# Kernel tuning notes

Hardware: AMD Instinct MI355X
Metric: run time of the kernel (lower is better)

The kernel has to match this reference:

```python
import jax, jax.numpy as jnp
import numpy as np

N = 100000
E = 1600000
IN_C, HID_C, OUT_C = 128, 64, 40


def setup_inputs() -> dict:
    key = jax.random.key(0)
    ks = jax.random.split(key, 9)
    x = jax.random.normal(ks[0], (N, IN_C), dtype=jnp.float32)
    src = jax.random.randint(ks[1], (E,), 0, N, dtype=jnp.int64)
    dst = jax.random.randint(ks[2], (E,), 0, N, dtype=jnp.int64)
    edge_index = jnp.stack([src, dst], axis=0)
    def glorot(k, fan_in, fan_out):
        s = jnp.sqrt(6.0 / (fan_in + fan_out)).astype(jnp.float32)
        return jax.random.uniform(k, (fan_in, fan_out), jnp.float32, -s, s)
    return {
        "x": x,
        "edge_index": edge_index,
        "W1": glorot(ks[3], IN_C, HID_C), "b1": jnp.zeros((HID_C,), jnp.float32),
        "W2": glorot(ks[4], HID_C, HID_C), "b2": jnp.zeros((HID_C,), jnp.float32),
        "W3": glorot(ks[5], HID_C, OUT_C), "b3": jnp.zeros((OUT_C,), jnp.float32),
    }


def _gcn_norm(edge_index, n_nodes):
    # add self-loops, then symmetric normalization D^-1/2 (A+I) D^-1/2
    loops = jnp.arange(n_nodes, dtype=edge_index.dtype)
    src = jnp.concatenate([edge_index[0], loops])
    dst = jnp.concatenate([edge_index[1], loops])
    deg = jax.ops.segment_sum(jnp.ones_like(dst, dtype=jnp.float32), dst,
                              num_segments=n_nodes)
    dinv = jnp.where(deg > 0, jax.lax.rsqrt(deg), 0.0)
    norm = dinv[src] * dinv[dst]  # [E + N]
    return src, dst, norm


def _gcn_conv(h, W, b, src, dst, norm, n_nodes):
    h = h @ W                                   # [N, out]
    msg = norm[:, None] * h[src]                # gather + scale, [E+N, out]
    out = jax.ops.segment_sum(msg, dst, num_segments=n_nodes)  # scatter-add
    return out + b


def reference(x, edge_index, W1, b1, W2, b2, W3, b3):
    n_nodes = x.shape[0]
    src, dst, norm = _gcn_norm(edge_index, n_nodes)
    h = jax.nn.relu(_gcn_conv(x, W1, b1, src, dst, norm, n_nodes))
    # dropout(p=0.5) is identity in eval mode
    h = jax.nn.relu(_gcn_conv(h, W2, b2, src, dst, norm, n_nodes))
    out = _gcn_conv(h, W3, b3, src, dst, norm, n_nodes)
    return out
```

## Files before the change

### kernel.cpp

```cpp
#include <hip/hip_runtime.h>

#define N_NODES 100000
#define N_EDGES 1600000
#define NBUCK 196
#define BCAP 9600
#define CH 4096
#define NCHUNK ((N_EDGES + CH - 1) / CH)

typedef __attribute__((ext_vector_type(2))) _Float16 half2v;
typedef __attribute__((ext_vector_type(4))) _Float16 half4v;

__device__ __forceinline__ float4 f4add(float4 a, float4 b) {
    return make_float4(a.x + b.x, a.y + b.y, a.z + b.z, a.w + b.w);
}
__device__ __forceinline__ float4 f4acch(float4 a, half4v v) {
    a.x += (float)v.x; a.y += (float)v.y; a.z += (float)v.z; a.w += (float)v.w;
    return a;
}


__global__ __launch_bounds__(256) void zero_small(int* p, int n) {
    int i = blockIdx.x * blockDim.x + threadIdx.x;
    if (i < n) p[i] = 0;
}

__global__ __launch_bounds__(256) void multisplit(const int* __restrict__ src,
                                                  const int* __restrict__ dst,
                                                  int* cursor,
                                                  int* __restrict__ bucketed, int e) {
    __shared__ int cnt[NBUCK];
    __shared__ int basel[NBUCK];
    const int t = threadIdx.x;
    const int base_e = blockIdx.x * CH;

    int myS[16], myD[16];
    for (int i = t; i < NBUCK; i += 256) cnt[i] = 0;
    __syncthreads();

#pragma unroll
    for (int k = 0; k < 16; ++k) {
        int i = base_e + k * 256 + t;
        if (i < e) {
            myS[k] = src[i];
            myD[k] = dst[i];
            atomicAdd(&cnt[myD[k] >> 9], 1);
        } else {
            myD[k] = -1;
        }
    }
    __syncthreads();
    for (int i = t; i < NBUCK; i += 256) basel[i] = atomicAdd(&cursor[i], cnt[i]);
    __syncthreads();
    for (int i = t; i < NBUCK; i += 256) cnt[i] = 0;
    __syncthreads();

#pragma unroll
    for (int k = 0; k < 16; ++k) {
        if (myD[k] >= 0) {
            int b = myD[k] >> 9;
            int pos = basel[b] + atomicAdd(&cnt[b], 1);
            if (pos < BCAP)
                bucketed[(size_t)b * BCAP + pos] = ((myD[k] & 511) << 17) | myS[k];
        }
    }
}

__global__ __launch_bounds__(256) void bucket_scan(const int* __restrict__ cursor,
                                                   int* __restrict__ gbase) {
    __shared__ int sm[256];
    const int t = threadIdx.x;
    int v = (t < NBUCK) ? cursor[t] : 0;
    sm[t] = v;
    __syncthreads();
    for (int off = 1; off < 256; off <<= 1) {
        int u = (t >= off) ? sm[t - off] : 0;
        __syncthreads();
        sm[t] += u;
        __syncthreads();
    }
    if (t < NBUCK) gbase[t] = sm[t] - v;
    if (t == NBUCK - 1) gbase[NBUCK] = sm[t];
}

__global__ __launch_bounds__(512) void build_csr(const int* __restrict__ bucketed,
                                                 const int* __restrict__ gbase,
                                                 int* __restrict__ row_ptr,
                                                 float* __restrict__ dinv,
                                                 int* __restrict__ csr_src, int n) {
    __shared__ int vals[BCAP];
    __shared__ int cnt[512];
    __shared__ int lcur[512];
    const int b = blockIdx.x;
    const int t = threadIdx.x;
    const int nb0 = b * 512;
    const int nn = min(512, n - nb0);
    const int gb = gbase[b];
    const int m = gbase[b + 1] - gb;

    cnt[t] = 0;
    __syncthreads();
    for (int i = t; i < m; i += 512) {
        int v = bucketed[(size_t)b * BCAP + i];
        vals[i] = v;
        atomicAdd(&cnt[v >> 17], 1);
    }
    __syncthreads();

    int deg = cnt[t];
    for (int off = 1; off < 512; off <<= 1) {
        int u = (t >= off) ? cnt[t - off] : 0;
        __syncthreads();
        cnt[t] += u;
        __syncthreads();
    }
    int offv = cnt[t] - deg;
    __syncthreads();
    cnt[t] = offv;
    lcur[t] = 0;
    if (t < nn) {
        row_ptr[nb0 + t] = gb + offv;
        dinv[nb0 + t] = rsqrtf((float)(deg + 1));
    }
    if (b == NBUCK - 1 && t == 0) row_ptr[n] = gb + m;
    __syncthreads();

    for (int i = t; i < m; i += 512) {
        int v = vals[i];
        int node = v >> 17;
        int pos = atomicAdd(&lcur[node], 1);
        csr_src[gb + cnt[node] + pos] = v & 0x1FFFF;
    }
}


template <int K, int COUT>
__global__ __launch_bounds__(256) void gemm_rt(const float* __restrict__ X,
                                               const float* __restrict__ W,
                                               const float* __restrict__ dinv,
                                               _Float16* __restrict__ Y, int n) {
    constexpr int KC = 64;
    constexpr int S = KC + 4;
    constexpr int NCHUNKK = K / KC;
    __shared__ float Xl[64 * S];
    __shared__ float Wl[KC * COUT];

    const int t = threadIdx.x;
    const int row0 = blockIdx.x * 64;
    const int cg = (t & 15) * 4;
    const int rg = (t >> 4) * 4;

    float acc[4][4] = {};

#pragma unroll
    for (int ch = 0; ch < NCHUNKK; ++ch) {
        const int k0 = ch * KC;
        for (int i = t; i < 64 * KC / 4; i += 256) {
            int r = i >> 4;
            int k = (i & 15) * 4;
            int grow = min(row0 + r, n - 1);
            *(float4*)(Xl + r * S + k) = *(const float4*)(X + (size_t)grow * K + k0 + k);
        }
        for (int i = t; i < KC * COUT / 4; i += 256) {
            *(float4*)(Wl + i * 4) = *(const float4*)(W + (size_t)k0 * COUT + (size_t)i * 4);
        }
        __syncthreads();

        if (cg < COUT) {
#pragma unroll 4
            for (int k = 0; k < KC; ++k) {
                float4 w = *(const float4*)(Wl + k * COUT + cg);
                float x0 = Xl[(rg + 0) * S + k];
                float x1 = Xl[(rg + 1) * S + k];
                float x2 = Xl[(rg + 2) * S + k];
                float x3 = Xl[(rg + 3) * S + k];
                acc[0][0] += x0 * w.x; acc[0][1] += x0 * w.y; acc[0][2] += x0 * w.z; acc[0][3] += x0 * w.w;
                acc[1][0] += x1 * w.x; acc[1][1] += x1 * w.y; acc[1][2] += x1 * w.z; acc[1][3] += x1 * w.w;
                acc[2][0] += x2 * w.x; acc[2][1] += x2 * w.y; acc[2][2] += x2 * w.z; acc[2][3] += x2 * w.w;
                acc[3][0] += x3 * w.x; acc[3][1] += x3 * w.y; acc[3][2] += x3 * w.z; acc[3][3] += x3 * w.w;
            }
        }
        __syncthreads();
    }

    if (cg < COUT) {
#pragma unroll
        for (int r = 0; r < 4; ++r) {
            int row = row0 + rg + r;
            if (row < n) {
                float d = dinv[row];
                half4v o = { (_Float16)(d * acc[r][0]), (_Float16)(d * acc[r][1]),
                             (_Float16)(d * acc[r][2]), (_Float16)(d * acc[r][3]) };
                *(half4v*)(Y + (size_t)row * COUT + cg) = o;
            }
        }
    }
}


template <bool RELU>
__global__ __launch_bounds__(256) void aggregate64v(const _Float16* __restrict__ tS,
                                                    const int* __restrict__ row_ptr,
                                                    const int* __restrict__ csr_src,
                                                    const float* __restrict__ dinv,
                                                    const float* __restrict__ bias,
                                                    float* __restrict__ out, int n) {
    const int lane = threadIdx.x & 63;
    const int node = blockIdx.x * 4 + (threadIdx.x >> 6);
    if (node >= n) return;
    const int g = lane >> 4;
    const int c4 = lane & 15;
    const half4v* tS4 = (const half4v*)tS;

    const int beg = row_ptr[node];
    const int cnt = row_ptr[node + 1] - beg;

    float4 a0 = {0,0,0,0}, a1 = {0,0,0,0}, a2 = {0,0,0,0}, a3 = {0,0,0,0};

    for (int j0 = 0; j0 < cnt; j0 += 64) {
        const int m = min(64, cnt - j0);
        int sj = (lane < m) ? csr_src[beg + j0 + lane] : 0;

        int j = 0;
        for (; j + 16 <= m; j += 16) {
            int e0 = __shfl(sj, j + g);
            int e1 = __shfl(sj, j + 4 + g);
            int e2 = __shfl(sj, j + 8 + g);
            int e3 = __shfl(sj, j + 12 + g);
            half4v v0 = tS4[(size_t)e0 * 16 + c4];
            half4v v1 = tS4[(size_t)e1 * 16 + c4];
            half4v v2 = tS4[(size_t)e2 * 16 + c4];
            half4v v3 = tS4[(size_t)e3 * 16 + c4];
            a0 = f4acch(a0, v0); a1 = f4acch(a1, v1);
            a2 = f4acch(a2, v2); a3 = f4acch(a3, v3);
        }
        for (; j + 4 <= m; j += 4) {
            int e0 = __shfl(sj, j + g);
            half4v v0 = tS4[(size_t)e0 * 16 + c4];
            a0 = f4acch(a0, v0);
        }
        if (j < m) {
            int idx = j + g;
            int e0 = __shfl(sj, idx < m ? idx : m - 1);
            half4v v = tS4[(size_t)e0 * 16 + c4];
            if (idx < m) a0 = f4acch(a0, v);
        }
    }

    float4 s = f4add(f4add(a0, a1), f4add(a2, a3));
#pragma unroll
    for (int off = 16; off < 64; off <<= 1) {
        s.x += __shfl_xor(s.x, off);
        s.y += __shfl_xor(s.y, off);
        s.z += __shfl_xor(s.z, off);
        s.w += __shfl_xor(s.w, off);
    }

    if (lane < 16) {
        half4v selfh = tS4[(size_t)node * 16 + c4];
        float4 b = ((const float4*)bias)[c4];
        float d = dinv[node];
        float4 o;
        o.x = b.x + d * (s.x + (float)selfh.x);
        o.y = b.y + d * (s.y + (float)selfh.y);
        o.z = b.z + d * (s.z + (float)selfh.z);
        o.w = b.w + d * (s.w + (float)selfh.w);
        if (RELU) {
            o.x = fmaxf(o.x, 0.f); o.y = fmaxf(o.y, 0.f);
            o.z = fmaxf(o.z, 0.f); o.w = fmaxf(o.w, 0.f);
        }
        ((float4*)out)[(size_t)node * 16 + c4] = o;
    }
}


__global__ __launch_bounds__(256) void aggregate40v(const _Float16* __restrict__ tS,
                                                    const int* __restrict__ row_ptr,
                                                    const int* __restrict__ csr_src,
                                                    const float* __restrict__ dinv,
                                                    const float* __restrict__ bias,
                                                    float* __restrict__ out, int n) {
    const int lane = threadIdx.x & 63;
    const int node = blockIdx.x * 4 + (threadIdx.x >> 6);
    if (node >= n) return;
    const int g = lane / 20;
    const int c2 = lane - 20 * g;
    const bool act = (g < 3);
    const half2v* tS2 = (const half2v*)tS;

    const int beg = row_ptr[node];
    const int cnt = row_ptr[node + 1] - beg;

    float2 a0 = {0,0}, a1 = {0,0}, a2 = {0,0}, a3 = {0,0};

    for (int j0 = 0; j0 < cnt; j0 += 64) {
        const int m = min(64, cnt - j0);
        int sj = (lane < m) ? csr_src[beg + j0 + lane] : 0;

        int j = 0;
        for (; j + 12 <= m; j += 12) {
            int i0 = j + g, i1 = j + 3 + g, i2 = j + 6 + g, i3 = j + 9 + g;
            int e0 = __shfl(sj, i0 < m ? i0 : 0);
            int e1 = __shfl(sj, i1 < m ? i1 : 0);
            int e2 = __shfl(sj, i2 < m ? i2 : 0);
            int e3 = __shfl(sj, i3 < m ? i3 : 0);
            half2v v0 = tS2[(size_t)e0 * 20 + c2];
            half2v v1 = tS2[(size_t)e1 * 20 + c2];
            half2v v2 = tS2[(size_t)e2 * 20 + c2];
            half2v v3 = tS2[(size_t)e3 * 20 + c2];
            if (act) {
                a0.x += (float)v0.x; a0.y += (float)v0.y;
                a1.x += (float)v1.x; a1.y += (float)v1.y;
                a2.x += (float)v2.x; a2.y += (float)v2.y;
                a3.x += (float)v3.x; a3.y += (float)v3.y;
            }
        }
        for (; j + 3 <= m; j += 3) {
            int i0 = j + g;
            int e0 = __shfl(sj, i0 < m ? i0 : 0);
            half2v v0 = tS2[(size_t)e0 * 20 + c2];
            if (act) { a0.x += (float)v0.x; a0.y += (float)v0.y; }
        }
        if (j < m) {
            int idx = j + g;
            int e0 = __shfl(sj, idx < m ? idx : m - 1);
            half2v v = tS2[(size_t)e0 * 20 + c2];
            if (act && idx < m) { a0.x += (float)v.x; a0.y += (float)v.y; }
        }
    }

    float2 s;
    s.x = (a0.x + a1.x) + (a2.x + a3.x);
    s.y = (a0.y + a1.y) + (a2.y + a3.y);
    float sx1 = __shfl(s.x, lane + 20), sy1 = __shfl(s.y, lane + 20);
    float sx2 = __shfl(s.x, lane + 40), sy2 = __shfl(s.y, lane + 40);
    if (lane < 20) {
        s.x += sx1 + sx2;
        s.y += sy1 + sy2;
        half2v selfh = tS2[(size_t)node * 20 + c2];
        float2 b = ((const float2*)bias)[c2];
        float d = dinv[node];
        float2 o;
        o.x = b.x + d * (s.x + (float)selfh.x);
        o.y = b.y + d * (s.y + (float)selfh.y);
        ((float2*)out)[(size_t)node * 20 + c2] = o;
    }
}


extern "C" void kernel_launch(void* const* d_in, const int* in_sizes, int n_in,
                              void* d_out, int out_size, void* d_ws, size_t ws_size,
                              hipStream_t stream) {
    const float* x  = (const float*)d_in[0];
    const int*   ei = (const int*)d_in[1];
    const int*   src = ei;
    const int*   dst = ei + N_EDGES;
    const float* W1 = (const float*)d_in[2];
    const float* b1 = (const float*)d_in[3];
    const float* W2 = (const float*)d_in[4];
    const float* b2 = (const float*)d_in[5];
    const float* W3 = (const float*)d_in[6];
    const float* b3 = (const float*)d_in[7];
    float* out = (float*)d_out;

    const int N = N_NODES, E = N_EDGES;

    char* p = (char*)d_ws;
    int*   cursor   = (int*)p;              p += 256 * 4;
    int*   gbase    = (int*)p;              p += 256 * 4;
    float* dinv     = (float*)p;            p += (size_t)N * 4;
    int*   row_ptr  = (int*)p;              p += (size_t)(N + 4) * 4;
    int*   bucketed = (int*)p;              p += (size_t)NBUCK * BCAP * 4;
    int*   csr_src  = (int*)p;              p += (size_t)E * 4;
    p = (char*)(((size_t)p + 15) & ~(size_t)15);
    _Float16* bufA  = (_Float16*)p;         p += (size_t)N * 64 * 2;
    p = (char*)(((size_t)p + 15) & ~(size_t)15);
    float*    bufB  = (float*)p;            p += (size_t)N * 64 * 4;

    zero_small<<<1, 256, 0, stream>>>(cursor, NBUCK);
    multisplit<<<NCHUNK, 256, 0, stream>>>(src, dst, cursor, bucketed, E);
    bucket_scan<<<1, 256, 0, stream>>>(cursor, gbase);
    build_csr<<<NBUCK, 512, 0, stream>>>(bucketed, gbase, row_ptr, dinv, csr_src, N);

    const int aggGrid = (N + 3) / 4;
    const int gemmGrid = (N + 63) / 64;

    gemm_rt<128, 64><<<gemmGrid, 256, 0, stream>>>(x, W1, dinv, bufA, N);
    aggregate64v<true><<<aggGrid, 256, 0, stream>>>(bufA, row_ptr, csr_src, dinv, b1, bufB, N);

    gemm_rt<64, 64><<<gemmGrid, 256, 0, stream>>>(bufB, W2, dinv, bufA, N);
    aggregate64v<true><<<aggGrid, 256, 0, stream>>>(bufA, row_ptr, csr_src, dinv, b2, bufB, N);

    gemm_rt<64, 40><<<gemmGrid, 256, 0, stream>>>(bufB, W3, dinv, bufA, N);
    aggregate40v<<<aggGrid, 256, 0, stream>>>(bufA, row_ptr, csr_src, dinv, b3, out, N);
}
```

Before: 349.9 us.

## Store hidden activations in fp16, widen aggregate gathers, transpose W in GEMM

```diff
diff --git a/kernel.cpp b/kernel.cpp
--- a/kernel.cpp
+++ b/kernel.cpp
@@ -9,13 +9,14 @@
 
 typedef __attribute__((ext_vector_type(2))) _Float16 half2v;
 typedef __attribute__((ext_vector_type(4))) _Float16 half4v;
-
-__device__ __forceinline__ float4 f4add(float4 a, float4 b) {
-    return make_float4(a.x + b.x, a.y + b.y, a.z + b.z, a.w + b.w);
-}
-__device__ __forceinline__ float4 f4acch(float4 a, half4v v) {
-    a.x += (float)v.x; a.y += (float)v.y; a.z += (float)v.z; a.w += (float)v.w;
-    return a;
+typedef __attribute__((ext_vector_type(8))) _Float16 half8v;
+
+__device__ __forceinline__ float4 loadX4(const float* X, size_t idx) {
+    return *(const float4*)(X + idx);
+}
+__device__ __forceinline__ float4 loadX4(const _Float16* X, size_t idx) {
+    half4v h = *(const half4v*)(X + idx);
+    return make_float4((float)h.x, (float)h.y, (float)h.z, (float)h.w);
 }
 
 
@@ -133,14 +134,86 @@
 }
 
 
-template <int K, int COUT>
-__global__ __launch_bounds__(256) void gemm_rt(const float* __restrict__ X,
+template <int K, typename XT>
+__global__ __launch_bounds__(256) void gemm64_rt(const XT* __restrict__ X,
+                                                 const float* __restrict__ W,
+                                                 const float* __restrict__ dinv,
+                                                 _Float16* __restrict__ Y, int n) {
+    constexpr int COUT = 64;
+    constexpr int KC = 64;
+    constexpr int S = KC + 4;
+    constexpr int NCH = K / KC;
+    __shared__ float Xl[64 * S];
+    __shared__ float Wt[64 * S];
+
+    const int t = threadIdx.x;
+    const int row0 = blockIdx.x * 64;
+    const int cg = (t & 15) * 4;
+    const int rg = (t >> 4) * 4;
+
+    float acc[4][4] = {};
+
+#pragma unroll
+    for (int ch = 0; ch < NCH; ++ch) {
+        const int k0 = ch * KC;
+        for (int i = t; i < 64 * KC / 4; i += 256) {
+            int r = i >> 4;
+            int k = (i & 15) * 4;
+            int grow = min(row0 + r, n - 1);
+            *(float4*)(Xl + r * S + k) = loadX4(X, (size_t)grow * K + k0 + k);
+        }
+        for (int i = t; i < KC * COUT; i += 256) {
+            int c = i & 63, k = i >> 6;
+            Wt[c * S + k] = W[(size_t)(k0 + k) * COUT + c];
+        }
+        __syncthreads();
+
+#pragma unroll 2
+        for (int k4 = 0; k4 < KC; k4 += 4) {
+            float4 xv0 = *(const float4*)(Xl + (rg + 0) * S + k4);
+            float4 xv1 = *(const float4*)(Xl + (rg + 1) * S + k4);
+            float4 xv2 = *(const float4*)(Xl + (rg + 2) * S + k4);
+            float4 xv3 = *(const float4*)(Xl + (rg + 3) * S + k4);
+            float4 wv0 = *(const float4*)(Wt + (cg + 0) * S + k4);
+            float4 wv1 = *(const float4*)(Wt + (cg + 1) * S + k4);
+            float4 wv2 = *(const float4*)(Wt + (cg + 2) * S + k4);
+            float4 wv3 = *(const float4*)(Wt + (cg + 3) * S + k4);
+            const float4 xv[4] = {xv0, xv1, xv2, xv3};
+            const float4 wv[4] = {wv0, wv1, wv2, wv3};
+#pragma unroll
+            for (int r = 0; r < 4; ++r)
+#pragma unroll
+                for (int c = 0; c < 4; ++c) {
+                    acc[r][c] += xv[r].x * wv[c].x;
+                    acc[r][c] += xv[r].y * wv[c].y;
+                    acc[r][c] += xv[r].z * wv[c].z;
+                    acc[r][c] += xv[r].w * wv[c].w;
+                }
+        }
+        __syncthreads();
+    }
+
+#pragma unroll
+    for (int r = 0; r < 4; ++r) {
+        int row = row0 + rg + r;
+        if (row < n) {
+            float d = dinv[row];
+            half4v o = { (_Float16)(d * acc[r][0]), (_Float16)(d * acc[r][1]),
+                         (_Float16)(d * acc[r][2]), (_Float16)(d * acc[r][3]) };
+            *(half4v*)(Y + (size_t)row * COUT + cg) = o;
+        }
+    }
+}
+
+
+template <int K, int COUT, typename XT>
+__global__ __launch_bounds__(256) void gemm_rt(const XT* __restrict__ X,
                                                const float* __restrict__ W,
                                                const float* __restrict__ dinv,
                                                _Float16* __restrict__ Y, int n) {
     constexpr int KC = 64;
     constexpr int S = KC + 4;
-    constexpr int NCHUNKK = K / KC;
+    constexpr int NCH = K / KC;
     __shared__ float Xl[64 * S];
     __shared__ float Wl[KC * COUT];
 
@@ -152,13 +225,13 @@
     float acc[4][4] = {};
 
 #pragma unroll
-    for (int ch = 0; ch < NCHUNKK; ++ch) {
+    for (int ch = 0; ch < NCH; ++ch) {
         const int k0 = ch * KC;
         for (int i = t; i < 64 * KC / 4; i += 256) {
             int r = i >> 4;
             int k = (i & 15) * 4;
             int grow = min(row0 + r, n - 1);
-            *(float4*)(Xl + r * S + k) = *(const float4*)(X + (size_t)grow * K + k0 + k);
+            *(float4*)(Xl + r * S + k) = loadX4(X, (size_t)grow * K + k0 + k);
         }
         for (int i = t; i < KC * COUT / 4; i += 256) {
             *(float4*)(Wl + i * 4) = *(const float4*)(W + (size_t)k0 * COUT + (size_t)i * 4);
@@ -198,77 +271,75 @@
 
 
 template <bool RELU>
-__global__ __launch_bounds__(256) void aggregate64v(const _Float16* __restrict__ tS,
+__global__ __launch_bounds__(256) void aggregate64b(const _Float16* __restrict__ tS,
                                                     const int* __restrict__ row_ptr,
                                                     const int* __restrict__ csr_src,
                                                     const float* __restrict__ dinv,
                                                     const float* __restrict__ bias,
-                                                    float* __restrict__ out, int n) {
+                                                    _Float16* __restrict__ out, int n) {
     const int lane = threadIdx.x & 63;
     const int node = blockIdx.x * 4 + (threadIdx.x >> 6);
     if (node >= n) return;
-    const int g = lane >> 4;
-    const int c4 = lane & 15;
-    const half4v* tS4 = (const half4v*)tS;
+    const int g = lane >> 3;
+    const int c8 = lane & 7;
+    const half8v* tS8 = (const half8v*)tS;
 
     const int beg = row_ptr[node];
     const int cnt = row_ptr[node + 1] - beg;
 
-    float4 a0 = {0,0,0,0}, a1 = {0,0,0,0}, a2 = {0,0,0,0}, a3 = {0,0,0,0};
+    float acc[8] = {};
 
     for (int j0 = 0; j0 < cnt; j0 += 64) {
         const int m = min(64, cnt - j0);
-        int sj = (lane < m) ? csr_src[beg + j0 + lane] : 0;
+        int sj = csr_src[beg + j0 + min(lane, m - 1)];
 
         int j = 0;
         for (; j + 16 <= m; j += 16) {
             int e0 = __shfl(sj, j + g);
-            int e1 = __shfl(sj, j + 4 + g);
-            int e2 = __shfl(sj, j + 8 + g);
-            int e3 = __shfl(sj, j + 12 + g);
-            half4v v0 = tS4[(size_t)e0 * 16 + c4];
-            half4v v1 = tS4[(size_t)e1 * 16 + c4];
-            half4v v2 = tS4[(size_t)e2 * 16 + c4];
-            half4v v3 = tS4[(size_t)e3 * 16 + c4];
-            a0 = f4acch(a0, v0); a1 = f4acch(a1, v1);
-            a2 = f4acch(a2, v2); a3 = f4acch(a3, v3);
-        }
-        for (; j + 4 <= m; j += 4) {
+            int e1 = __shfl(sj, j + 8 + g);
+            half8v v0 = tS8[(size_t)e0 * 8 + c8];
+            half8v v1 = tS8[(size_t)e1 * 8 + c8];
+#pragma unroll
+            for (int i = 0; i < 8; ++i) acc[i] += (float)v0[i];
+#pragma unroll
+            for (int i = 0; i < 8; ++i) acc[i] += (float)v1[i];
+        }
+        for (; j + 8 <= m; j += 8) {
             int e0 = __shfl(sj, j + g);
-            half4v v0 = tS4[(size_t)e0 * 16 + c4];
-            a0 = f4acch(a0, v0);
+            half8v v0 = tS8[(size_t)e0 * 8 + c8];
+#pragma unroll
+            for (int i = 0; i < 8; ++i) acc[i] += (float)v0[i];
         }
         if (j < m) {
             int idx = j + g;
-            int e0 = __shfl(sj, idx < m ? idx : m - 1);
-            half4v v = tS4[(size_t)e0 * 16 + c4];
-            if (idx < m) a0 = f4acch(a0, v);
-        }
-    }
-
-    float4 s = f4add(f4add(a0, a1), f4add(a2, a3));
-#pragma unroll
-    for (int off = 16; off < 64; off <<= 1) {
-        s.x += __shfl_xor(s.x, off);
-        s.y += __shfl_xor(s.y, off);
-        s.z += __shfl_xor(s.z, off);
-        s.w += __shfl_xor(s.w, off);
-    }
-
-    if (lane < 16) {
-        half4v selfh = tS4[(size_t)node * 16 + c4];
-        float4 b = ((const float4*)bias)[c4];
+            int e0 = __shfl(sj, min(idx, m - 1));
+            half8v v = tS8[(size_t)e0 * 8 + c8];
+            float flag = (idx < m) ? 1.0f : 0.0f;
+#pragma unroll
+            for (int i = 0; i < 8; ++i) acc[i] = fmaf(flag, (float)v[i], acc[i]);
+        }
+    }
+
+#pragma unroll
+    for (int off = 8; off < 64; off <<= 1) {
+#pragma unroll
+        for (int i = 0; i < 8; ++i) acc[i] += __shfl_xor(acc[i], off);
+    }
+
+    if (lane < 8) {
+        half8v selfh = tS8[(size_t)node * 8 + c8];
+        float4 b0 = *(const float4*)(bias + c8 * 8);
+        float4 b1 = *(const float4*)(bias + c8 * 8 + 4);
+        const float bb[8] = {b0.x, b0.y, b0.z, b0.w, b1.x, b1.y, b1.z, b1.w};
         float d = dinv[node];
-        float4 o;
-        o.x = b.x + d * (s.x + (float)selfh.x);
-        o.y = b.y + d * (s.y + (float)selfh.y);
-        o.z = b.z + d * (s.z + (float)selfh.z);
-        o.w = b.w + d * (s.w + (float)selfh.w);
-        if (RELU) {
-            o.x = fmaxf(o.x, 0.f); o.y = fmaxf(o.y, 0.f);
-            o.z = fmaxf(o.z, 0.f); o.w = fmaxf(o.w, 0.f);
-        }
-        ((float4*)out)[(size_t)node * 16 + c4] = o;
+        half8v o;
+#pragma unroll
+        for (int i = 0; i < 8; ++i) {
+            float v = bb[i] + d * (acc[i] + (float)selfh[i]);
+            if (RELU) v = fmaxf(v, 0.0f);
+            o[i] = (_Float16)v;
+        }
+        ((half8v*)out)[(size_t)node * 8 + c8] = o;
     }
 }
 
@@ -374,7 +445,7 @@
     p = (char*)(((size_t)p + 15) & ~(size_t)15);
     _Float16* bufA  = (_Float16*)p;         p += (size_t)N * 64 * 2;
     p = (char*)(((size_t)p + 15) & ~(size_t)15);
-    float*    bufB  = (float*)p;            p += (size_t)N * 64 * 4;
+    _Float16* bufB  = (_Float16*)p;         p += (size_t)N * 64 * 2;
 
     zero_small<<<1, 256, 0, stream>>>(cursor, NBUCK);
     multisplit<<<NCHUNK, 256, 0, stream>>>(src, dst, cursor, bucketed, E);
@@ -384,12 +455,12 @@
     const int aggGrid = (N + 3) / 4;
     const int gemmGrid = (N + 63) / 64;
 
-    gemm_rt<128, 64><<<gemmGrid, 256, 0, stream>>>(x, W1, dinv, bufA, N);
-    aggregate64v<true><<<aggGrid, 256, 0, stream>>>(bufA, row_ptr, csr_src, dinv, b1, bufB, N);
-
-    gemm_rt<64, 64><<<gemmGrid, 256, 0, stream>>>(bufB, W2, dinv, bufA, N);
-    aggregate64v<true><<<aggGrid, 256, 0, stream>>>(bufA, row_ptr, csr_src, dinv, b2, bufB, N);
-
-    gemm_rt<64, 40><<<gemmGrid, 256, 0, stream>>>(bufB, W3, dinv, bufA, N);
+    gemm64_rt<128, float><<<gemmGrid, 256, 0, stream>>>(x, W1, dinv, bufA, N);
+    aggregate64b<true><<<aggGrid, 256, 0, stream>>>(bufA, row_ptr, csr_src, dinv, b1, bufB, N);
+
+    gemm64_rt<64, _Float16><<<gemmGrid, 256, 0, stream>>>(bufB, W2, dinv, bufA, N);
+    aggregate64b<true><<<aggGrid, 256, 0, stream>>>(bufA, row_ptr, csr_src, dinv, b2, bufB, N);
+
+    gemm_rt<64, 40, _Float16><<<gemmGrid, 256, 0, stream>>>(bufB, W3, dinv, bufA, N);
     aggregate40v<<<aggGrid, 256, 0, stream>>>(bufA, row_ptr, csr_src, dinv, b3, out, N);
 }
```

After: 367.3 us. 5.0% more time.
